# Optimization experiments

Hardware: AMD Instinct MI355X
Metric: run time of the kernel (lower is better)

## Reference

```python
import jax, jax.numpy as jnp
import numpy as np

SRC_LEN, TRG_LEN, BATCH, HID_DIM, ATT_DIM = 256, 256, 32, 512, 128


def setup_inputs() -> dict:
    key = jax.random.key(0)
    k1, k2, k3, k4, k5, k6 = jax.random.split(key, 6)
    dec_out = jax.random.normal(k1, (TRG_LEN, BATCH, HID_DIM), dtype=jnp.float32)
    enc_outs = jax.random.normal(k2, (SRC_LEN, BATCH, HID_DIM), dtype=jnp.float32)
    # Linear weights (scaled like kaiming-ish init so tanh isn't saturated)
    W_s = jax.random.normal(k3, (ATT_DIM, HID_DIM), dtype=jnp.float32) / np.sqrt(HID_DIM)
    W_t = jax.random.normal(k4, (ATT_DIM, HID_DIM), dtype=jnp.float32) / np.sqrt(HID_DIM)
    b_t = jax.random.normal(k5, (ATT_DIM,), dtype=jnp.float32) * 0.01
    # v_a ~ U(-0.05, 0.05), shape (att_dim, 1) as in the torch module
    v_a = jax.random.uniform(k6, (ATT_DIM, 1), dtype=jnp.float32, minval=-0.05, maxval=0.05)
    return {"dec_out": dec_out, "enc_outs": enc_outs, "W_s": W_s, "W_t": W_t, "b_t": b_t, "v_a": v_a}


def reference(dec_out, enc_outs, W_s, W_t, b_t, v_a):
    # enc projection: (src, batch, hid) -> (src, batch, att)
    enc_att = jnp.einsum('sbh,ah->sba', enc_outs, W_s)
    # dec projection (with bias): (trg, batch, hid) -> (trg, batch, att)
    dec_att = jnp.einsum('tbh,ah->tba', dec_out, W_t) + b_t
    # broadcast-add + tanh: (src, trg, batch, att), then reduce with v_a
    dec_enc = jnp.tanh(enc_att[:, None, :, :] + dec_att[None, :, :, :])
    scores = jnp.einsum('stba,a->tbs', dec_enc, v_a[:, 0])  # (trg, batch, src)
    return scores
```

## Files before the change

kernel.cpp:

```cpp
#include <hip/hip_runtime.h>

#define SRC_LEN 256
#define TRG_LEN 256
#define BATCH   32
#define HID     512
#define ATT     128
#define CSCALE  2.885390081777927f

typedef float  f32x4  __attribute__((ext_vector_type(4)));
typedef short  bf16x8 __attribute__((ext_vector_type(8)));

__device__ inline unsigned short bfr(float x) {
    unsigned u = __builtin_bit_cast(unsigned, x);
    return (unsigned short)((u + 0x7fffu + ((u >> 16) & 1u)) >> 16);
}
__device__ inline unsigned pk2(float a, float b) {
    return (unsigned)bfr(a) | ((unsigned)bfr(b) << 16);
}

__global__ __launch_bounds__(256) void prep_kernel(
    const float* __restrict__ W_s, const float* __restrict__ W_t,
    const float* __restrict__ v_a,
    uint4* __restrict__ Wb, float* __restrict__ sumvP)
{
    const int blk = blockIdx.x;
    if (blk < 16) {
        const int iw = blk >> 3, a_tile = blk & 7;
        const float* __restrict__ W = iw ? W_t : W_s;
        uint4* __restrict__ dst = Wb + ((size_t)iw * 8 + a_tile) * 1024;
        #pragma unroll
        for (int oo = 0; oo < 4; ++oo) {
            const int o = threadIdx.x + oo * 256;
            const int c = o >> 7, rem = o & 127;
            const int s = rem >> 6, lane = rem & 63;
            const int q = lane >> 4, l15 = lane & 15;
            const int row = a_tile * 16 + l15;
            const int k0 = c * 64 + s * 32 + q * 8;
            const float4 f0 = *(const float4*)(W + (size_t)row * HID + k0);
            const float4 f1 = *(const float4*)(W + (size_t)row * HID + k0 + 4);
            uint4 u;
            u.x = pk2(f0.x, f0.y); u.y = pk2(f0.z, f0.w);
            u.z = pk2(f1.x, f1.y); u.w = pk2(f1.z, f1.w);
            dst[o] = u;
        }
    } else {
        const int tid = threadIdx.x;
        float x = 0.f;
        if (tid < 64) x = v_a[tid] + v_a[tid + 64];
        #pragma unroll
        for (int o = 32; o > 0; o >>= 1) x += __shfl_down(x, o);
        if (tid == 0) *sumvP = x;
    }
}

__global__ __launch_bounds__(256, 4) void proj_mfma(
    const float* __restrict__ dec_out, const float* __restrict__ enc_outs,
    const float* __restrict__ b_t, const uint4* __restrict__ Wb,
    float* __restrict__ encE, float* __restrict__ decD)
{
    __shared__ __align__(16) char smem[8704];

    const int tid   = threadIdx.x;
    const int blk   = blockIdx.x;
    const bool isDec = blk >= 512;
    const int blkL  = isDec ? blk - 512 : blk;
    const int bb    = blkL & 31;
    const int r0    = (blkL >> 5) * 16;
    const float* __restrict__ in = isDec ? dec_out : enc_outs;
    const uint4* __restrict__ Wk = Wb + (isDec ? 8192 : 0);

    const int lane = tid & 63;
    const int w    = tid >> 6;
    const int woff_n = w * 32;
    const int q = lane >> 4, l15 = lane & 15, l7 = lane & 7;

    const int srow = tid >> 4;
    const int skc  = tid & 15;
    const int sg   = skc >> 1, shalf = skc & 1;
    const float* aGp = in + ((size_t)(r0 + srow) * BATCH + bb) * HID + skc * 4;

    float4 aR;
    f32x4 acc[2];
    acc[0] = (f32x4)0.0f;
    acc[1] = (f32x4)0.0f;

    #define LOADG(c) { aR = *(const float4*)(aGp + (size_t)(c) * 64); }
    #define STORES(buf)                                                      \
        {                                                                    \
            char* ab = smem + (buf) * 2048;                                  \
            uint2 u;                                                         \
            u.x = pk2(aR.x, aR.y);                                           \
            u.y = pk2(aR.z, aR.w);                                           \
            *(uint2*)(ab + srow * 128 + ((sg ^ (srow & 7)) << 4)             \
                      + shalf * 8) = u;                                      \
        }

    LOADG(0);
    STORES(0);
    __syncthreads();

    for (int c = 0; c < 8; ++c) {
        if (c < 7) LOADG(c + 1);
        const char* ab = smem + (c & 1) * 2048;
        #pragma unroll
        for (int s = 0; s < 2; ++s) {
            bf16x8 af = *(const bf16x8*)(ab + l15 * 128
                                         + (((s * 4 + q) ^ l7) << 4));
            #pragma unroll
            for (int ni = 0; ni < 2; ++ni) {
                const int a_tile = w * 2 + ni;
                bf16x8 bfv = *(const bf16x8*)(Wk + (((a_tile * 8 + c) * 2 + s) * 64 + lane));
                acc[ni] = __builtin_amdgcn_mfma_f32_16x16x32_bf16(
                    af, bfv, acc[ni], 0, 0, 0);
            }
        }
        if (c < 7) STORES((c + 1) & 1);
        __syncthreads();
    }

    if (!isDec) {
        float* T = (float*)smem;
        #pragma unroll
        for (int ni = 0; ni < 2; ++ni)
            #pragma unroll
            for (int r = 0; r < 4; ++r) {
                const int ml = q * 4 + r;
                const int nl = woff_n + ni * 16 + l15;
                T[ml * 132 + nl] = __builtin_amdgcn_exp2f(-CSCALE * acc[ni][r]);
            }
        __syncthreads();
        {
            const int m  = tid & 15;
            const int g0 = tid >> 4;
            #pragma unroll
            for (int p = 0; p < 2; ++p) {
                const int gq = g0 + p * 16;
                float4 v = *(const float4*)(T + m * 132 + gq * 4);
                *(float4*)(encE + (((size_t)bb * 32 + gq) * SRC_LEN + r0 + m) * 4) = v;
            }
        }
    } else {
        float bt[2];
        bt[0] = b_t[woff_n + l15];
        bt[1] = b_t[woff_n + 16 + l15];
        #pragma unroll
        for (int ni = 0; ni < 2; ++ni)
            #pragma unroll
            for (int r = 0; r < 4; ++r) {
                const int ml = q * 4 + r;
                const int nl = woff_n + ni * 16 + l15;
                decD[((size_t)(r0 + ml) * BATCH + bb) * ATT + nl] =
                    __builtin_amdgcn_exp2f(CSCALE * (acc[ni][r] + bt[ni]));
            }
    }
    #undef LOADG
    #undef STORES
}

__global__ __launch_bounds__(256) void score_kernel(
    const float* __restrict__ encE, const float* __restrict__ decD,
    const float* __restrict__ v_a, const float* __restrict__ sumvP,
    float* __restrict__ out)
{
    const int tid = threadIdx.x;
    const int t0  = blockIdx.x * 4;
    const int b   = blockIdx.y;

    float acc0 = 0.f, acc1 = 0.f, acc2 = 0.f, acc3 = 0.f;
    const float* __restrict__ ep = encE + ((size_t)b * 32 * SRC_LEN + tid) * 4;
    const float* __restrict__ dBase = decD + ((size_t)t0 * BATCH + b) * ATT;

    #pragma unroll
    for (int g = 0; g < 32; ++g) {
        const float4 E  = *(const float4*)(ep + (size_t)g * SRC_LEN * 4);
        const float4 vv = *(const float4*)(v_a + g * 4);
        const float n0 = vv.x * E.x, n1 = vv.y * E.y;
        const float n2 = vv.z * E.z, n3 = vv.w * E.w;

        #define TSTEP(ACC, TT)                                             \
        {                                                                  \
            const float4 d = *(const float4*)(dBase                        \
                + (size_t)(TT) * BATCH * ATT + g * 4);         \
            const float x0 = E.x + d.x, x1 = E.y + d.y;                    \
            const float x2 = E.z + d.z, x3 = E.w + d.w;                    \
            const float a01 = x0 * x1, a23 = x2 * x3;                      \
            const float den = a01 * a23;                                   \
            const float m01 = fmaf(n0, x1, n1 * x0);                       \
            const float m23 = fmaf(n2, x3, n3 * x2);                       \
            const float num = fmaf(m01, a23, m23 * a01);                   \
            ACC = fmaf(num, __builtin_amdgcn_rcpf(den), ACC);              \
        }
        TSTEP(acc0, 0)
        TSTEP(acc1, 1)
        TSTEP(acc2, 2)
        TSTEP(acc3, 3)
        #undef TSTEP
    }

    const float sv = *sumvP;
    out[((size_t)(t0 + 0) * BATCH + b) * SRC_LEN + tid] = sv - 2.0f * acc0;
    out[((size_t)(t0 + 1) * BATCH + b) * SRC_LEN + tid] = sv - 2.0f * acc1;
    out[((size_t)(t0 + 2) * BATCH + b) * SRC_LEN + tid] = sv - 2.0f * acc2;
    out[((size_t)(t0 + 3) * BATCH + b) * SRC_LEN + tid] = sv - 2.0f * acc3;
}

extern "C" void kernel_launch(void* const* d_in, const int* in_sizes, int n_in,
                              void* d_out, int out_size, void* d_ws, size_t ws_size,
                              hipStream_t stream) {
    const float* dec_out  = (const float*)d_in[0];
    const float* enc_outs = (const float*)d_in[1];
    const float* W_s      = (const float*)d_in[2];
    const float* W_t      = (const float*)d_in[3];
    const float* b_t      = (const float*)d_in[4];
    const float* v_a      = (const float*)d_in[5];
    float* out = (float*)d_out;

    float* encE = (float*)d_ws;
    float* decD = encE + (size_t)BATCH * ATT * SRC_LEN;
    uint4* Wb   = (uint4*)(decD + (size_t)TRG_LEN * BATCH * ATT);
    float* sumvP = (float*)(Wb + 2 * 8192);

    prep_kernel<<<17, 256, 0, stream>>>(W_s, W_t, v_a, Wb, sumvP);
    proj_mfma<<<1024, 256, 0, stream>>>(dec_out, enc_outs, b_t, Wb, encE, decD);
    score_kernel<<<dim3(TRG_LEN / 4, BATCH), 256, 0, stream>>>(encE, decD, v_a, sumvP, out);
}
```

Measured before the change: 123.1 us.

## Reformulate tanh scoring via product form, stage dec tile in LDS, drop A staging

The score kernel now stores exp(2x) of the encoder projection instead of exp(-2x), so each term becomes 1+E*D with fmaf and the per-g v*E products are removed. Decoder rows and v_a are staged in shared memory, and the v_a sum moves into the score kernel, which drops a prep block. The projection kernel now loads A directly from global into registers and converts it to bf16 there, replacing the double-buffered LDS path and its barriers. The grid order is swapped so batch varies fastest. Risks include overflow of the product form for large activations and less coalesced A loads without LDS staging.

After: 126.4 us. 2.6% more time.

```diff
diff --git a/kernel.cpp b/kernel.cpp
--- a/kernel.cpp
+++ b/kernel.cpp
@@ -20,36 +20,26 @@
 
 __global__ __launch_bounds__(256) void prep_kernel(
     const float* __restrict__ W_s, const float* __restrict__ W_t,
-    const float* __restrict__ v_a,
-    uint4* __restrict__ Wb, float* __restrict__ sumvP)
+    uint4* __restrict__ Wb)
 {
     const int blk = blockIdx.x;
-    if (blk < 16) {
-        const int iw = blk >> 3, a_tile = blk & 7;
-        const float* __restrict__ W = iw ? W_t : W_s;
-        uint4* __restrict__ dst = Wb + ((size_t)iw * 8 + a_tile) * 1024;
-        #pragma unroll
-        for (int oo = 0; oo < 4; ++oo) {
-            const int o = threadIdx.x + oo * 256;
-            const int c = o >> 7, rem = o & 127;
-            const int s = rem >> 6, lane = rem & 63;
-            const int q = lane >> 4, l15 = lane & 15;
-            const int row = a_tile * 16 + l15;
-            const int k0 = c * 64 + s * 32 + q * 8;
-            const float4 f0 = *(const float4*)(W + (size_t)row * HID + k0);
-            const float4 f1 = *(const float4*)(W + (size_t)row * HID + k0 + 4);
-            uint4 u;
-            u.x = pk2(f0.x, f0.y); u.y = pk2(f0.z, f0.w);
-            u.z = pk2(f1.x, f1.y); u.w = pk2(f1.z, f1.w);
-            dst[o] = u;
-        }
-    } else {
-        const int tid = threadIdx.x;
-        float x = 0.f;
-        if (tid < 64) x = v_a[tid] + v_a[tid + 64];
-        #pragma unroll
-        for (int o = 32; o > 0; o >>= 1) x += __shfl_down(x, o);
-        if (tid == 0) *sumvP = x;
+    const int iw = blk >> 3, a_tile = blk & 7;
+    const float* __restrict__ W = iw ? W_t : W_s;
+    uint4* __restrict__ dst = Wb + ((size_t)iw * 8 + a_tile) * 1024;
+    #pragma unroll
+    for (int oo = 0; oo < 4; ++oo) {
+        const int o = threadIdx.x + oo * 256;
+        const int c = o >> 7, rem = o & 127;
+        const int s = rem >> 6, lane = rem & 63;
+        const int q = lane >> 4, l15 = lane & 15;
+        const int row = a_tile * 16 + l15;
+        const int k0 = c * 64 + s * 32 + q * 8;
+        const float4 f0 = *(const float4*)(W + (size_t)row * HID + k0);
+        const float4 f1 = *(const float4*)(W + (size_t)row * HID + k0 + 4);
+        uint4 u;
+        u.x = pk2(f0.x, f0.y); u.y = pk2(f0.z, f0.w);
+        u.z = pk2(f1.x, f1.y); u.w = pk2(f1.z, f1.w);
+        dst[o] = u;
     }
 }
 
@@ -58,7 +48,7 @@
     const float* __restrict__ b_t, const uint4* __restrict__ Wb,
     float* __restrict__ encE, float* __restrict__ decD)
 {
-    __shared__ __align__(16) char smem[8704];
+    __shared__ __align__(16) float T[16 * 132];
 
     const int tid   = threadIdx.x;
     const int blk   = blockIdx.x;
@@ -72,61 +62,45 @@
     const int lane = tid & 63;
     const int w    = tid >> 6;
     const int woff_n = w * 32;
-    const int q = lane >> 4, l15 = lane & 15, l7 = lane & 7;
-
-    const int srow = tid >> 4;
-    const int skc  = tid & 15;
-    const int sg   = skc >> 1, shalf = skc & 1;
-    const float* aGp = in + ((size_t)(r0 + srow) * BATCH + bb) * HID + skc * 4;
-
-    float4 aR;
+    const int q = lane >> 4, l15 = lane & 15;
+
+    const float* __restrict__ aBase =
+        in + ((size_t)(r0 + l15) * BATCH + bb) * HID + q * 8;
+
     f32x4 acc[2];
     acc[0] = (f32x4)0.0f;
     acc[1] = (f32x4)0.0f;
 
-    #define LOADG(c) { aR = *(const float4*)(aGp + (size_t)(c) * 64); }
-    #define STORES(buf)                                                      \
-        {                                                                    \
-            char* ab = smem + (buf) * 2048;                                  \
-            uint2 u;                                                         \
-            u.x = pk2(aR.x, aR.y);                                           \
-            u.y = pk2(aR.z, aR.w);                                           \
-            *(uint2*)(ab + srow * 128 + ((sg ^ (srow & 7)) << 4)             \
-                      + shalf * 8) = u;                                      \
-        }
-
-    LOADG(0);
-    STORES(0);
-    __syncthreads();
-
+    #pragma unroll
     for (int c = 0; c < 8; ++c) {
-        if (c < 7) LOADG(c + 1);
-        const char* ab = smem + (c & 1) * 2048;
         #pragma unroll
         for (int s = 0; s < 2; ++s) {
-            bf16x8 af = *(const bf16x8*)(ab + l15 * 128
-                                         + (((s * 4 + q) ^ l7) << 4));
+            const int k = c * 64 + s * 32;
+            const float4 f0 = *(const float4*)(aBase + k);
+            const float4 f1 = *(const float4*)(aBase + k + 4);
+            uint4 ua;
+            ua.x = pk2(f0.x, f0.y); ua.y = pk2(f0.z, f0.w);
+            ua.z = pk2(f1.x, f1.y); ua.w = pk2(f1.z, f1.w);
+            const bf16x8 af = __builtin_bit_cast(bf16x8, ua);
             #pragma unroll
             for (int ni = 0; ni < 2; ++ni) {
                 const int a_tile = w * 2 + ni;
-                bf16x8 bfv = *(const bf16x8*)(Wk + (((a_tile * 8 + c) * 2 + s) * 64 + lane));
+                const bf16x8 bfv = *(const bf16x8*)(
+                    Wk + (((a_tile * 8 + c) * 2 + s) * 64 + lane));
                 acc[ni] = __builtin_amdgcn_mfma_f32_16x16x32_bf16(
                     af, bfv, acc[ni], 0, 0, 0);
             }
         }
-        if (c < 7) STORES((c + 1) & 1);
-        __syncthreads();
     }
 
     if (!isDec) {
-        float* T = (float*)smem;
         #pragma unroll
         for (int ni = 0; ni < 2; ++ni)
             #pragma unroll
             for (int r = 0; r < 4; ++r) {
                 const int ml = q * 4 + r;
                 const int nl = woff_n + ni * 16 + l15;
-                T[ml * 132 + nl] = __builtin_amdgcn_exp2f(-CSCALE * acc[ni][r]);
+                T[ml * 132 + nl] = __builtin_amdgcn_exp2f(CSCALE * acc[ni][r]);
             }
         __syncthreads();
         {
@@ -153,51 +127,67 @@
                     __builtin_amdgcn_exp2f(CSCALE * (acc[ni][r] + bt[ni]));
             }
     }
-    #undef LOADG
-    #undef STORES
 }
 
 __global__ __launch_bounds__(256) void score_kernel(
     const float* __restrict__ encE, const float* __restrict__ decD,
-    const float* __restrict__ v_a, const float* __restrict__ sumvP,
-    float* __restrict__ out)
+    const float* __restrict__ v_a, float* __restrict__ out)
 {
+    __shared__ float dS[4 * ATT];
+    __shared__ float vS[ATT];
+    __shared__ float sumvS;
+
     const int tid = threadIdx.x;
-    const int t0  = blockIdx.x * 4;
-    const int b   = blockIdx.y;
+    const int b   = blockIdx.x;
+    const int t0  = blockIdx.y * 4;
+
+    if (tid < 128) {
+        const int tt = tid >> 5, a4 = (tid & 31) * 4;
+        *(float4*)(dS + tt * ATT + a4) =
+            *(const float4*)(decD + ((size_t)(t0 + tt) * BATCH + b) * ATT + a4);
+    } else if (tid < 160) {
+        const int l = tid - 128;
+        *(float4*)(vS + l * 4) = *(const float4*)(v_a + l * 4);
+    }
+    __syncthreads();
+    if (tid < 64) {
+        float x = vS[tid] + vS[tid + 64];
+        #pragma unroll
+        for (int o = 32; o > 0; o >>= 1) x += __shfl_down(x, o);
+        if (tid == 0) sumvS = x;
+    }
+    __syncthreads();
 
     float acc0 = 0.f, acc1 = 0.f, acc2 = 0.f, acc3 = 0.f;
     const float* __restrict__ ep = encE + ((size_t)b * 32 * SRC_LEN + tid) * 4;
-    const float* __restrict__ dBase = decD + ((size_t)t0 * BATCH + b) * ATT;
 
     #pragma unroll
     for (int g = 0; g < 32; ++g) {
-        const float4 E  = *(const float4*)(ep + (size_t)g * SRC_LEN * 4);
-        const float4 vv = *(const float4*)(v_a + g * 4);
-        const float n0 = vv.x * E.x, n1 = vv.y * E.y;
-        const float n2 = vv.z * E.z, n3 = vv.w * E.w;
-
-        #define TSTEP(ACC, TT)                                             \
+        const float4 F  = *(const float4*)(ep + (size_t)g * SRC_LEN * 4);
+        const float4 vv = *(const float4*)(vS + g * 4);
+
+        #define TSTEP(ACC, DBASE)                                          \
         {                                                                  \
-            const float4 d = *(const float4*)(dBase                        \
-                + (size_t)(TT) * BATCH * ATT + g * 4);         \
-            const float x0 = E.x + d.x, x1 = E.y + d.y;                    \
-            const float x2 = E.z + d.z, x3 = E.w + d.w;                    \
-            const float a01 = x0 * x1, a23 = x2 * x3;                      \
+            const float4 d = *(const float4*)(DBASE + g * 4);              \
+            const float y0 = fmaf(F.x, d.x, 1.0f);                         \
+            const float y1 = fmaf(F.y, d.y, 1.0f);                         \
+            const float y2 = fmaf(F.z, d.z, 1.0f);                         \
+            const float y3 = fmaf(F.w, d.w, 1.0f);                         \
+            const float a01 = y0 * y1, a23 = y2 * y3;                      \
             const float den = a01 * a23;                                   \
-            const float m01 = fmaf(n0, x1, n1 * x0);                       \
-            const float m23 = fmaf(n2, x3, n3 * x2);                       \
+            const float m01 = fmaf(vv.x, y1, vv.y * y0);                   \
+            const float m23 = fmaf(vv.z, y3, vv.w * y2);                   \
             const float num = fmaf(m01, a23, m23 * a01);                   \
             ACC = fmaf(num, __builtin_amdgcn_rcpf(den), ACC);              \
         }
-        TSTEP(acc0, 0)
-        TSTEP(acc1, 1)
-        TSTEP(acc2, 2)
-        TSTEP(acc3, 3)
+        TSTEP(acc0, dS + 0 * ATT)
+        TSTEP(acc1, dS + 1 * ATT)
+        TSTEP(acc2, dS + 2 * ATT)
+        TSTEP(acc3, dS + 3 * ATT)
         #undef TSTEP
     }
 
-    const float sv = *sumvP;
+    const float sv = sumvS;
     out[((size_t)(t0 + 0) * BATCH + b) * SRC_LEN + tid] = sv - 2.0f * acc0;
     out[((size_t)(t0 + 1) * BATCH + b) * SRC_LEN + tid] = sv - 2.0f * acc1;
     out[((size_t)(t0 + 2) * BATCH + b) * SRC_LEN + tid] = sv - 2.0f * acc2;
@@ -218,9 +208,8 @@
     float* encE = (float*)d_ws;
     float* decD = encE + (size_t)BATCH * ATT * SRC_LEN;
     uint4* Wb   = (uint4*)(decD + (size_t)TRG_LEN * BATCH * ATT);
-    float* sumvP = (float*)(Wb + 2 * 8192);
-
-    prep_kernel<<<17, 256, 0, stream>>>(W_s, W_t, v_a, Wb, sumvP);
+
+    prep_kernel<<<16, 256, 0, stream>>>(W_s, W_t, Wb);
     proj_mfma<<<1024, 256, 0, stream>>>(dec_out, enc_outs, b_t, Wb, encE, decD);
-    score_kernel<<<dim3(TRG_LEN / 4, BATCH), 256, 0, stream>>>(encE, decD, v_a, sumvP, out);
-}
+    score_kernel<<<dim3(BATCH, TRG_LEN / 4), 256, 0, stream>>>(encE, decD, v_a, out);
+}
```
